# Kernel optimization log

Measured on AMD Instinct MI355X. Metric: run time of the kernel, lower is better.

The kernel has to match this reference:

```python
import jax, jax.numpy as jnp
import numpy as np

B, T, E, NH = 2, 1024, 512, 8


def setup_inputs() -> dict:
    key = jax.random.key(0)
    ks = jax.random.split(key, 7)
    s = 0.02
    return {
        "x": jax.random.normal(ks[0], (B, T, E), dtype=jnp.float32),
        "W_qkv": jax.random.normal(ks[1], (E, 3 * E), dtype=jnp.float32) * s,
        "b_qkv": jax.random.normal(ks[2], (3 * E,), dtype=jnp.float32) * s,
        "W_od": jax.random.normal(ks[3], (E, 2 * NH), dtype=jnp.float32) * s,
        "b_od": jax.random.normal(ks[4], (2 * NH,), dtype=jnp.float32) * s,
        "W_out": jax.random.normal(ks[5], (E, E), dtype=jnp.float32) * s,
        "b_out": jax.random.normal(ks[6], (E,), dtype=jnp.float32) * s,
        "length": T,
    }


def reference(x, W_qkv, b_qkv, W_od, b_od, W_out, b_out, length):
    b, t, e = x.shape
    nh = W_od.shape[1] // 2
    hd = e // nh
    scaling = float(hd) ** (-0.5)

    qkv = x @ W_qkv + b_qkv
    Q, K, V = jnp.split(qkv, 3, axis=-1)  # each (b, t, e)

    od = Q @ W_od + b_od  # (b, t, 2*nh)
    offset, duration = jnp.split(od, 2, axis=-1)
    offset = jnp.tanh(offset) * length
    duration = jax.nn.sigmoid(duration) * length

    qidx = jnp.arange(length, dtype=x.dtype)[None, :, None]  # (1, t, 1)
    anchor = qidx + offset  # (b, t, nh)

    # 'b t nh -> (b nh) t'
    anchor = anchor.transpose(0, 2, 1).reshape(b * nh, t)
    duration = duration.transpose(0, 2, 1).reshape(b * nh, t)

    start = anchor - duration
    end = anchor + duration
    bl = jnp.floor(start)          # left bound index
    br = jnp.ceil(end)             # right bound index
    al = jnp.floor(anchor)         # anchor left index
    ar = al + 1                    # anchor right index
    dist_al = anchor - al          # anchor_dist_l

    r = jnp.arange(length, dtype=x.dtype)[None, None, :]  # (1, 1, t)

    def pmask(idx):  # point mask (bnh, t, t), float
        return (r == idx[:, :, None]).astype(x.dtype)

    point_weight = (1.0
                    + (bl - start)[:, :, None] * pmask(bl)
                    + (end - br)[:, :, None] * pmask(br)
                    + dist_al[:, :, None] * pmask(ar)
                    + (1.0 - dist_al)[:, :, None] * pmask(al))

    attn_mask = (r < bl[:, :, None]) | (r > br[:, :, None])  # (bnh, t, t) bool

    def heads(z):  # 'b t (nh hd) -> (b nh) t hd'
        return z.reshape(b, t, nh, hd).transpose(0, 2, 1, 3).reshape(b * nh, t, hd)

    Qh, Kh, Vh = heads(Q), heads(K), heads(V)

    scores = jnp.einsum('bic,brc->bir', Qh, Kh) * scaling
    scores = scores * point_weight
    scores = jnp.where(attn_mask, jnp.asarray(-1e8, x.dtype), scores)
    attn = jax.nn.softmax(scores, axis=-1)

    out = jnp.einsum('bir,brc->bic', attn, Vh)  # (bnh, t, hd)
    out = out.reshape(b, nh, t, hd).transpose(0, 2, 1, 3).reshape(b, t, e)
    return out @ W_out + b_out
```

## Files before the change

### kernel.cpp

```cpp
#include <hip/hip_runtime.h>

typedef unsigned short ushort_t;
typedef short s16x8 __attribute__((ext_vector_type(8)));
typedef float f32x4 __attribute__((ext_vector_type(4)));

#define DEVINL __device__ __forceinline__

DEVINL ushort_t f2b(float f) {
  union { float f; unsigned int u; } v; v.f = f;
  unsigned int r = (v.u + 0x7fffu + ((v.u >> 16) & 1u)) >> 16;
  return (ushort_t)r;
}

DEVINL ushort_t f2b_hw(float f) {
  union { __bf16 h; ushort_t u; } cv;
  cv.h = (__bf16)f;
  return cv.u;
}

__global__ __launch_bounds__(256) void prep_kernel(
    const float* __restrict__ Wqkv, const float* __restrict__ bq,
    const float* __restrict__ Wod, const float* __restrict__ bod,
    const float* __restrict__ Wout,
    ushort_t* __restrict__ WqkvT, ushort_t* __restrict__ WoT,
    float* __restrict__ Wcomb, float* __restrict__ bcomb)
{
  __shared__ ushort_t tile[64 * 72];
  const int b = blockIdx.x;
  const int tid = threadIdx.x;

  if (b < 256) {
    const float* in;
    ushort_t* out;
    int N, bx, by;
    if (b < 192) { in = Wqkv; out = WqkvT; N = 1536; bx = b % 24; by = b / 24; }
    else         { in = Wout; out = WoT;   N = 512;  bx = (b - 192) % 8; by = (b - 192) / 8; }
    const int K = 512;
    const int n0 = bx * 64, k0 = by * 64;
    const int cr = tid >> 4;
    const int cc = (tid & 15) * 4;
#pragma unroll
    for (int p = 0; p < 4; p++) {
      int k = k0 + p * 16 + cr;
      float4 v = *(const float4*)(in + k * N + n0 + cc);
      ushort4 o; o.x = f2b(v.x); o.y = f2b(v.y); o.z = f2b(v.z); o.w = f2b(v.w);
      *(ushort4*)(tile + (p * 16 + cr) * 72 + cc) = o;
    }
    __syncthreads();
#pragma unroll
    for (int p = 0; p < 4; p++) {
      int n = n0 + p * 16 + cr;
      ushort4 v;
      v.x = tile[(cc + 0) * 72 + p * 16 + cr];
      v.y = tile[(cc + 1) * 72 + p * 16 + cr];
      v.z = tile[(cc + 2) * 72 + p * 16 + cr];
      v.w = tile[(cc + 3) * 72 + p * 16 + cr];
      *(ushort4*)(out + n * K + k0 + cc) = v;
    }
    return;
  }

  const int w = tid >> 6, lane = tid & 63;
  const int c = (b - 256) * 4 + w;
  if (c > 512) return;
  float a[8];
  const float* src = (c < 512) ? (Wqkv + c * 1536 + lane * 8) : (bq + lane * 8);
  float4 a0 = *(const float4*)(src);
  float4 a1 = *(const float4*)(src + 4);
  a[0]=a0.x; a[1]=a0.y; a[2]=a0.z; a[3]=a0.w;
  a[4]=a1.x; a[5]=a1.y; a[6]=a1.z; a[7]=a1.w;

  float s[16];
#pragma unroll
  for (int j = 0; j < 16; j++) s[j] = 0.f;
#pragma unroll
  for (int i = 0; i < 8; i++) {
    const float* wp = Wod + (lane * 8 + i) * 16;
#pragma unroll
    for (int j = 0; j < 16; j++) s[j] += a[i] * wp[j];
  }
#pragma unroll
  for (int mask = 1; mask < 64; mask <<= 1)
#pragma unroll
    for (int j = 0; j < 16; j++) s[j] += __shfl_xor(s[j], mask);

  if (lane < 16) {
    if (c < 512) Wcomb[c * 16 + lane] = s[lane];
    else         bcomb[lane] = s[lane] + bod[lane];
  }
}

__global__ __launch_bounds__(256) void od_kernel(
    const float* __restrict__ x, const float* __restrict__ Wcomb,
    const float* __restrict__ bcomb, const int* __restrict__ lenp,
    float* __restrict__ params, ushort_t* __restrict__ xb)
{
  const int w = threadIdx.x >> 6, lane = threadIdx.x & 63;
  const int m = blockIdx.x * 4 + w;
  int li = lenp[0];
  float len = (li > 0 && li < 1048576) ? (float)li : 1024.0f;

  const float* qp = x + m * 512 + lane * 8;
  float q[8];
  float4 qa = *(const float4*)(qp);
  float4 qb = *(const float4*)(qp + 4);
  q[0]=qa.x; q[1]=qa.y; q[2]=qa.z; q[3]=qa.w;
  q[4]=qb.x; q[5]=qb.y; q[6]=qb.z; q[7]=qb.w;

  s16x8 ov;
#pragma unroll
  for (int i = 0; i < 8; i++) ov[i] = (short)f2b(q[i]);
  *(s16x8*)(xb + m * 512 + lane * 8) = ov;

  float s[16];
#pragma unroll
  for (int j = 0; j < 16; j++) s[j] = 0.f;
#pragma unroll
  for (int i = 0; i < 8; i++) {
    const float* wp = Wcomb + (lane * 8 + i) * 16;
#pragma unroll
    for (int j = 0; j < 16; j++) s[j] += q[i] * wp[j];
  }
#pragma unroll
  for (int mask = 1; mask < 64; mask <<= 1)
#pragma unroll
    for (int j = 0; j < 16; j++) s[j] += __shfl_xor(s[j], mask);

  if (lane < 8) {
    int h = lane;
    int bb = m >> 10, t = m & 1023;
    float odo = s[h] + bcomb[h];
    float odd = s[8 + h] + bcomb[8 + h];
    float offset = tanhf(odo) * len;
    float dur = len / (1.f + expf(-odd));
    float anchor = (float)t + offset;
    float start = anchor - dur, end = anchor + dur;
    float bl = floorf(start), br = ceilf(end);
    float al = floorf(anchor);
    float da = anchor - al;
    float* pp = params + ((bb * 8 + h) * 1024 + t) * 6;
    pp[0] = bl; pp[1] = br; pp[2] = al;
    pp[3] = bl - start; pp[4] = end - br; pp[5] = da;
  }
}

__global__ __launch_bounds__(256) void qkv_gemm_kernel(
    const ushort_t* __restrict__ xb, const ushort_t* __restrict__ WT,
    const float* __restrict__ bqkv,
    ushort_t* __restrict__ Qh, ushort_t* __restrict__ Kh, ushort_t* __restrict__ VT)
{
  __shared__ ushort_t As[64 * 32];
  __shared__ ushort_t Bs[128 * 32];
  const int tid = threadIdx.x;
  const int lane = tid & 63, w = tid >> 6;
  const int wr = w >> 1, wc = w & 1;
  const int quad = lane >> 4, l16 = lane & 15;
  const int m0 = blockIdx.y * 64, n0 = blockIdx.x * 128;

  f32x4 acc[2][4];
#pragma unroll
  for (int i = 0; i < 2; i++)
#pragma unroll
    for (int j = 0; j < 4; j++) acc[i][j] = f32x4{0.f, 0.f, 0.f, 0.f};

  const int idx = tid * 8;
  const int ra = idx >> 5, ca = idx & 31;
  const int rb1 = (idx + 2048) >> 5, cb1 = (idx + 2048) & 31;

  for (int k0 = 0; k0 < 512; k0 += 32) {
    s16x8 va  = *(const s16x8*)(xb + (m0 + ra) * 512 + k0 + ca);
    s16x8 vb0 = *(const s16x8*)(WT + (n0 + ra) * 512 + k0 + ca);
    s16x8 vb1 = *(const s16x8*)(WT + (n0 + rb1) * 512 + k0 + cb1);
    __syncthreads();
    *(s16x8*)(As + idx) = va;
    *(s16x8*)(Bs + idx) = vb0;
    *(s16x8*)(Bs + idx + 2048) = vb1;
    __syncthreads();

    s16x8 af[2], bfr[4];
#pragma unroll
    for (int mt = 0; mt < 2; mt++)
      af[mt] = *(const s16x8*)(As + (wr * 32 + mt * 16 + l16) * 32 + quad * 8);
#pragma unroll
    for (int nt = 0; nt < 4; nt++)
      bfr[nt] = *(const s16x8*)(Bs + (wc * 64 + nt * 16 + l16) * 32 + quad * 8);
#pragma unroll
    for (int mt = 0; mt < 2; mt++)
#pragma unroll
      for (int nt = 0; nt < 4; nt++)
        acc[mt][nt] = __builtin_amdgcn_mfma_f32_16x16x32_bf16(af[mt], bfr[nt], acc[mt][nt], 0, 0, 0);
  }

#pragma unroll
  for (int nt = 0; nt < 4; nt++) {
    int c = n0 + wc * 64 + nt * 16 + l16;
    float bias = bqkv[c];
    int which = c >> 9;
    int e = c & 511;
    int h = e >> 6, d = e & 63;
#pragma unroll
    for (int mt = 0; mt < 2; mt++) {
      int mbase = m0 + wr * 32 + mt * 16 + quad * 4;
      int bb = mbase >> 10, t = mbase & 1023;
      int bh = bb * 8 + h;
      if (which == 2) {
        ushort4 pk;
        pk.x = f2b(acc[mt][nt][0] + bias);
        pk.y = f2b(acc[mt][nt][1] + bias);
        pk.z = f2b(acc[mt][nt][2] + bias);
        pk.w = f2b(acc[mt][nt][3] + bias);
        *(ushort4*)(VT + (bh * 64 + d) * 1024 + t) = pk;
      } else {
        ushort_t* dst = (which == 0) ? Qh : Kh;
        float sc = (which == 0) ? 0.125f : 1.0f;
#pragma unroll
        for (int rr = 0; rr < 4; rr++)
          dst[(bh * 1024 + t + rr) * 64 + d] = f2b((acc[mt][nt][rr] + bias) * sc);
      }
    }
  }
}

__global__ __launch_bounds__(256, 3) void attn_kernel(
    const ushort_t* __restrict__ Qh, const ushort_t* __restrict__ Kh,
    const ushort_t* __restrict__ VT, const float* __restrict__ params,
    ushort_t* __restrict__ Oh)
{
  __shared__ ushort_t Kt[64 * 72 + 32];
  __shared__ ushort_t Vt[64 * 72 + 96];
  __shared__ ushort_t Ps[4][16 * 40];
  __shared__ float Om[4][16][65];
  __shared__ float lwS[4][16];

  const int tid = threadIdx.x;
  const int lane = tid & 63, w = tid >> 6;
  const int quad = lane >> 4, l16 = lane & 15;
  const int bh = blockIdx.x;
  const int mrow = blockIdx.y * 16;
  ushort_t* Pw = Ps[w];

#pragma unroll
  for (int rr = 0; rr < 4; rr++)
    Pw[(quad * 4 + rr) * 40 + 16 + l16] = 0;

  s16x8 aq0 = *(const s16x8*)(Qh + (bh * 1024 + mrow + l16) * 64 + quad * 8);
  s16x8 aq1 = *(const s16x8*)(Qh + (bh * 1024 + mrow + l16) * 64 + 32 + quad * 8);

  float bl[4], br[4], al[4], wl[4], wr2[4], da[4];
  float lo = 1.0e9f, hi = -1.0e9f;
#pragma unroll
  for (int rr = 0; rr < 4; rr++) {
    int row = mrow + quad * 4 + rr;
    const float* pp = params + (bh * 1024 + row) * 6;
    bl[rr] = pp[0]; br[rr] = pp[1]; al[rr] = pp[2];
    wl[rr] = pp[3]; wr2[rr] = pp[4]; da[rr] = pp[5];
    bool empty = (br[rr] < 0.f) || (bl[rr] > 1023.f);
    float lo_r = empty ? 0.f    : fmaxf(bl[rr], 0.f);
    float hi_r = empty ? 1023.f : fminf(br[rr], 1023.f);
    lo = fminf(lo, lo_r); hi = fmaxf(hi, hi_r);
  }
  lo = fminf(lo, __shfl_xor(lo, 16));
  lo = fminf(lo, __shfl_xor(lo, 32));
  hi = fmaxf(hi, __shfl_xor(hi, 16));
  hi = fmaxf(hi, __shfl_xor(hi, 32));
  const int tlo = ((int)lo) >> 6, thi = ((int)hi) >> 6;

  float lr[4] = {0.f, 0.f, 0.f, 0.f};
  f32x4 Oacc[4];
#pragma unroll
  for (int nt = 0; nt < 4; nt++) Oacc[nt] = f32x4{0.f, 0.f, 0.f, 0.f};

  const int srow = tid >> 2, sseg = (tid & 3) * 16;
  const ushort_t* kgb = Kh + (bh * 1024 + srow) * 64 + sseg;
  const ushort_t* vgb = VT + (bh * 64 + srow) * 1024 + sseg;

  s16x8 kr0, kr1, vr0, vr1;
  {
    const int r0 = tlo * 64;
    kr0 = *(const s16x8*)(kgb + r0 * 64);
    kr1 = *(const s16x8*)(kgb + r0 * 64 + 8);
    vr0 = *(const s16x8*)(vgb + r0);
    vr1 = *(const s16x8*)(vgb + r0 + 8);
  }

  for (int tt = tlo; tt <= thi; tt++) {
    const int r0 = tt * 64;
    __syncthreads();
    *(s16x8*)(Kt + srow * 72 + sseg)     = kr0;
    *(s16x8*)(Kt + srow * 72 + sseg + 8) = kr1;
    *(s16x8*)(Vt + srow * 72 + sseg)     = vr0;
    *(s16x8*)(Vt + srow * 72 + sseg + 8) = vr1;
    __syncthreads();

    if (tt + 1 <= thi) {
      const int r1 = (tt + 1) * 64;
      kr0 = *(const s16x8*)(kgb + r1 * 64);
      kr1 = *(const s16x8*)(kgb + r1 * 64 + 8);
      vr0 = *(const s16x8*)(vgb + r1);
      vr1 = *(const s16x8*)(vgb + r1 + 8);
    }

    s16x8 bk0 = *(const s16x8*)(Kt + (w * 16 + l16) * 72 + quad * 8);
    s16x8 bk1 = *(const s16x8*)(Kt + (w * 16 + l16) * 72 + 32 + quad * 8);
    f32x4 S = {0.f, 0.f, 0.f, 0.f};
    S = __builtin_amdgcn_mfma_f32_16x16x32_bf16(aq0, bk0, S, 0, 0, 0);
    S = __builtin_amdgcn_mfma_f32_16x16x32_bf16(aq1, bk1, S, 0, 0, 0);

    const float cf = (float)(r0 + w * 16 + l16);
    const float c0f = (float)(r0 + w * 16), c1f = c0f + 15.f;
    bool fastb = true;
#pragma unroll
    for (int rr = 0; rr < 4; rr++) {
      bool f = (bl[rr] < c0f) && (br[rr] > c1f) &&
               ((al[rr] + 1.f < c0f) || (al[rr] > c1f));
      fastb = fastb && f;
    }
    float p4[4];
    if (__all((int)fastb)) {
#pragma unroll
      for (int rr = 0; rr < 4; rr++) {
        float p = __expf(S[rr]);
        lr[rr] += p;
        p4[rr] = p;
      }
    } else {
#pragma unroll
      for (int rr = 0; rr < 4; rr++) {
        float s = S[rr];
        float wgt = 1.f;
        wgt += (cf == bl[rr]) ? wl[rr] : 0.f;
        wgt += (cf == br[rr]) ? wr2[rr] : 0.f;
        wgt += (cf == al[rr] + 1.f) ? da[rr] : 0.f;
        wgt += (cf == al[rr]) ? (1.f - da[rr]) : 0.f;
        s *= wgt;
        s = (cf < bl[rr] || cf > br[rr]) ? -30.f : s;
        float p = __expf(s);
        lr[rr] += p;
        p4[rr] = p;
      }
    }

#pragma unroll
    for (int rr = 0; rr < 4; rr++)
      Pw[(quad * 4 + rr) * 40 + l16] = f2b_hw(p4[rr]);

    s16x8 pa = *(const s16x8*)(Pw + l16 * 40 + quad * 8);
#pragma unroll
    for (int nt = 0; nt < 4; nt++) {
      s16x8 bv = *(const s16x8*)(Vt + (nt * 16 + l16) * 72 + w * 16 + quad * 8);
      Oacc[nt] = __builtin_amdgcn_mfma_f32_16x16x32_bf16(pa, bv, Oacc[nt], 0, 0, 0);
    }
  }

#pragma unroll
  for (int mask = 1; mask < 16; mask <<= 1)
#pragma unroll
    for (int rr = 0; rr < 4; rr++) lr[rr] += __shfl_xor(lr[rr], mask);

#pragma unroll
  for (int nt = 0; nt < 4; nt++)
#pragma unroll
    for (int rr = 0; rr < 4; rr++)
      Om[w][quad * 4 + rr][nt * 16 + l16] = Oacc[nt][rr];
  if (l16 == 0) {
#pragma unroll
    for (int rr = 0; rr < 4; rr++) lwS[w][quad * 4 + rr] = lr[rr];
  }
  __syncthreads();

  {
    const int col = tid & 63;
    const int rbase = (tid >> 6) * 4;
    const int bb = bh >> 3, h = bh & 7;
#pragma unroll
    for (int k = 0; k < 4; k++) {
      int r = rbase + k;
      float lg = lwS[0][r] + lwS[1][r] + lwS[2][r] + lwS[3][r];
      float o  = Om[0][r][col] + Om[1][r][col] + Om[2][r][col] + Om[3][r][col];
      int t = mrow + r;
      Oh[((bb << 10) + t) * 512 + h * 64 + col] = f2b_hw(o / lg);
    }
  }
}

__global__ __launch_bounds__(256) void out_gemm_kernel(
    const ushort_t* __restrict__ Oh, const ushort_t* __restrict__ WT,
    const float* __restrict__ bout, float* __restrict__ outp)
{
  __shared__ ushort_t As[64 * 32];
  __shared__ ushort_t Bs[64 * 32];
  const int tid = threadIdx.x;
  const int lane = tid & 63, w = tid >> 6;
  const int wr = w >> 1, wc = w & 1;
  const int quad = lane >> 4, l16 = lane & 15;
  const int m0 = blockIdx.y * 64, n0 = blockIdx.x * 64;

  f32x4 acc[2][2];
#pragma unroll
  for (int i = 0; i < 2; i++)
#pragma unroll
    for (int j = 0; j < 2; j++) acc[i][j] = f32x4{0.f, 0.f, 0.f, 0.f};

  const int idx = tid * 8;
  const int ra = idx >> 5, ca = idx & 31;

  for (int k0 = 0; k0 < 512; k0 += 32) {
    s16x8 va = *(const s16x8*)(Oh + (m0 + ra) * 512 + k0 + ca);
    s16x8 vb = *(const s16x8*)(WT + (n0 + ra) * 512 + k0 + ca);
    __syncthreads();
    *(s16x8*)(As + idx) = va;
    *(s16x8*)(Bs + idx) = vb;
    __syncthreads();

    s16x8 af[2], bfr[2];
#pragma unroll
    for (int mt = 0; mt < 2; mt++)
      af[mt] = *(const s16x8*)(As + (wr * 32 + mt * 16 + l16) * 32 + quad * 8);
#pragma unroll
    for (int nt = 0; nt < 2; nt++)
      bfr[nt] = *(const s16x8*)(Bs + (wc * 32 + nt * 16 + l16) * 32 + quad * 8);
#pragma unroll
    for (int mt = 0; mt < 2; mt++)
#pragma unroll
      for (int nt = 0; nt < 2; nt++)
        acc[mt][nt] = __builtin_amdgcn_mfma_f32_16x16x32_bf16(af[mt], bfr[nt], acc[mt][nt], 0, 0, 0);
  }

#pragma unroll
  for (int nt = 0; nt < 2; nt++) {
    int c = n0 + wc * 32 + nt * 16 + l16;
    float bias = bout[c];
#pragma unroll
    for (int mt = 0; mt < 2; mt++) {
#pragma unroll
      for (int rr = 0; rr < 4; rr++) {
        int m = m0 + wr * 32 + mt * 16 + quad * 4 + rr;
        outp[m * 512 + c] = acc[mt][nt][rr] + bias;
      }
    }
  }
}

extern "C" void kernel_launch(void* const* d_in, const int* in_sizes, int n_in,
                              void* d_out, int out_size, void* d_ws, size_t ws_size,
                              hipStream_t stream)
{
  const float* x    = (const float*)d_in[0];
  const float* Wqkv = (const float*)d_in[1];
  const float* bqkv = (const float*)d_in[2];
  const float* Wod  = (const float*)d_in[3];
  const float* bod  = (const float*)d_in[4];
  const float* Wout = (const float*)d_in[5];
  const float* bout = (const float*)d_in[6];
  const int* lenp   = (const int*)d_in[7];

  char* ws = (char*)d_ws;
  ushort_t* WqkvT  = (ushort_t*)(ws);
  ushort_t* WoT    = (ushort_t*)(ws + 1572864);
  ushort_t* xb     = (ushort_t*)(ws + 2097152);
  ushort_t* Qh     = (ushort_t*)(ws + 4194304);
  ushort_t* Kh     = (ushort_t*)(ws + 6291456);
  ushort_t* VT     = (ushort_t*)(ws + 8388608);
  ushort_t* Oh     = (ushort_t*)(ws + 10485760);
  float*    Wcomb  = (float*)(ws + 12582912);
  float*    bcomb  = (float*)(ws + 12615680);
  float*    params = (float*)(ws + 12615744);

  prep_kernel<<<385, 256, 0, stream>>>(Wqkv, bqkv, Wod, bod, Wout, WqkvT, WoT, Wcomb, bcomb);
  od_kernel<<<512, 256, 0, stream>>>(x, Wcomb, bcomb, lenp, params, xb);
  qkv_gemm_kernel<<<dim3(12, 32), 256, 0, stream>>>(xb, WqkvT, bqkv, Qh, Kh, VT);
  attn_kernel<<<dim3(16, 64), 256, 0, stream>>>(Qh, Kh, VT, params, Oh);
  out_gemm_kernel<<<dim3(8, 32), 256, 0, stream>>>(Oh, WoT, bout, (float*)d_out);
}
```

Before: 129.9 us.

## Double-buffer K/V tiles and process 32 query rows per attention block

```diff
diff --git a/kernel.cpp b/kernel.cpp
--- a/kernel.cpp
+++ b/kernel.cpp
@@ -226,31 +226,27 @@
     const ushort_t* __restrict__ VT, const float* __restrict__ params,
     ushort_t* __restrict__ Oh)
 {
-  __shared__ ushort_t Kt[64 * 72 + 32];
-  __shared__ ushort_t Vt[64 * 72 + 96];
+  constexpr int TS = 64 * 72;
+  __shared__ __align__(16) ushort_t KV[4 * TS];
   __shared__ ushort_t Ps[4][16 * 40];
-  __shared__ float Om[4][16][65];
-  __shared__ float lwS[4][16];
+  __shared__ float loS[4], hiS[4];
 
   const int tid = threadIdx.x;
   const int lane = tid & 63, w = tid >> 6;
+  const int wr = w >> 1, wc = w & 1;
   const int quad = lane >> 4, l16 = lane & 15;
   const int bh = blockIdx.x;
-  const int mrow = blockIdx.y * 16;
+  const int mrow = blockIdx.y * 32;
   ushort_t* Pw = Ps[w];
 
-#pragma unroll
-  for (int rr = 0; rr < 4; rr++)
-    Pw[(quad * 4 + rr) * 40 + 16 + l16] = 0;
-
-  s16x8 aq0 = *(const s16x8*)(Qh + (bh * 1024 + mrow + l16) * 64 + quad * 8);
-  s16x8 aq1 = *(const s16x8*)(Qh + (bh * 1024 + mrow + l16) * 64 + 32 + quad * 8);
+  s16x8 aq0 = *(const s16x8*)(Qh + (bh * 1024 + mrow + wr * 16 + l16) * 64 + quad * 8);
+  s16x8 aq1 = *(const s16x8*)(Qh + (bh * 1024 + mrow + wr * 16 + l16) * 64 + 32 + quad * 8);
 
   float bl[4], br[4], al[4], wl[4], wr2[4], da[4];
   float lo = 1.0e9f, hi = -1.0e9f;
 #pragma unroll
   for (int rr = 0; rr < 4; rr++) {
-    int row = mrow + quad * 4 + rr;
+    int row = mrow + wr * 16 + quad * 4 + rr;
     const float* pp = params + (bh * 1024 + row) * 6;
     bl[rr] = pp[0]; br[rr] = pp[1]; al[rr] = pp[2];
     wl[rr] = pp[3]; wr2[rr] = pp[4]; da[rr] = pp[5];
@@ -263,6 +259,10 @@
   lo = fminf(lo, __shfl_xor(lo, 32));
   hi = fmaxf(hi, __shfl_xor(hi, 16));
   hi = fmaxf(hi, __shfl_xor(hi, 32));
+  if (lane == 0) { loS[w] = lo; hiS[w] = hi; }
+  __syncthreads();
+  lo = fminf(fminf(loS[0], loS[1]), fminf(loS[2], loS[3]));
+  hi = fmaxf(fmaxf(hiS[0], hiS[1]), fmaxf(hiS[2], hiS[3]));
   const int tlo = ((int)lo) >> 6, thi = ((int)hi) >> 6;
 
   float lr[4] = {0.f, 0.f, 0.f, 0.f};
@@ -282,17 +282,24 @@
     vr0 = *(const s16x8*)(vgb + r0);
     vr1 = *(const s16x8*)(vgb + r0 + 8);
   }
-
-  for (int tt = tlo; tt <= thi; tt++) {
-    const int r0 = tt * 64;
-    __syncthreads();
+  {
+    ushort_t* Kt = KV;
+    ushort_t* Vt = KV + TS;
     *(s16x8*)(Kt + srow * 72 + sseg)     = kr0;
     *(s16x8*)(Kt + srow * 72 + sseg + 8) = kr1;
     *(s16x8*)(Vt + srow * 72 + sseg)     = vr0;
     *(s16x8*)(Vt + srow * 72 + sseg + 8) = vr1;
-    __syncthreads();
-
-    if (tt + 1 <= thi) {
+  }
+  __syncthreads();
+
+  for (int tt = tlo; tt <= thi; tt++) {
+    const int p = (tt - tlo) & 1;
+    ushort_t* Ktp = KV + p * 2 * TS;
+    ushort_t* Vtp = KV + p * 2 * TS + TS;
+    const int r0 = tt * 64;
+    const bool more = (tt + 1 <= thi);
+
+    if (more) {
       const int r1 = (tt + 1) * 64;
       kr0 = *(const s16x8*)(kgb + r1 * 64);
       kr1 = *(const s16x8*)(kgb + r1 * 64 + 8);
@@ -300,14 +307,20 @@
       vr1 = *(const s16x8*)(vgb + r1 + 8);
     }
 
-    s16x8 bk0 = *(const s16x8*)(Kt + (w * 16 + l16) * 72 + quad * 8);
-    s16x8 bk1 = *(const s16x8*)(Kt + (w * 16 + l16) * 72 + 32 + quad * 8);
-    f32x4 S = {0.f, 0.f, 0.f, 0.f};
-    S = __builtin_amdgcn_mfma_f32_16x16x32_bf16(aq0, bk0, S, 0, 0, 0);
-    S = __builtin_amdgcn_mfma_f32_16x16x32_bf16(aq1, bk1, S, 0, 0, 0);
-
-    const float cf = (float)(r0 + w * 16 + l16);
-    const float c0f = (float)(r0 + w * 16), c1f = c0f + 15.f;
+    f32x4 S[2];
+#pragma unroll
+    for (int ng = 0; ng < 2; ng++) {
+      const ushort_t* kp = Ktp + (wc * 32 + ng * 16 + l16) * 72 + quad * 8;
+      s16x8 bk0 = *(const s16x8*)(kp);
+      s16x8 bk1 = *(const s16x8*)(kp + 32);
+      f32x4 z = {0.f, 0.f, 0.f, 0.f};
+      z = __builtin_amdgcn_mfma_f32_16x16x32_bf16(aq0, bk0, z, 0, 0, 0);
+      z = __builtin_amdgcn_mfma_f32_16x16x32_bf16(aq1, bk1, z, 0, 0, 0);
+      S[ng] = z;
+    }
+
+    const int cbase = r0 + wc * 32;
+    const float c0f = (float)cbase, c1f = c0f + 31.f;
     bool fastb = true;
 #pragma unroll
     for (int rr = 0; rr < 4; rr++) {
@@ -315,71 +328,89 @@
                ((al[rr] + 1.f < c0f) || (al[rr] > c1f));
       fastb = fastb && f;
     }
-    float p4[4];
+    float p8[2][4];
     if (__all((int)fastb)) {
 #pragma unroll
-      for (int rr = 0; rr < 4; rr++) {
-        float p = __expf(S[rr]);
-        lr[rr] += p;
-        p4[rr] = p;
+      for (int ng = 0; ng < 2; ng++)
+#pragma unroll
+        for (int rr = 0; rr < 4; rr++) {
+          float pv = __expf(S[ng][rr]);
+          lr[rr] += pv;
+          p8[ng][rr] = pv;
+        }
+    } else {
+#pragma unroll
+      for (int ng = 0; ng < 2; ng++) {
+        const float cf = (float)(cbase + ng * 16 + l16);
+#pragma unroll
+        for (int rr = 0; rr < 4; rr++) {
+          float s = S[ng][rr];
+          float wgt = 1.f;
+          wgt += (cf == bl[rr]) ? wl[rr] : 0.f;
+          wgt += (cf == br[rr]) ? wr2[rr] : 0.f;
+          wgt += (cf == al[rr] + 1.f) ? da[rr] : 0.f;
+          wgt += (cf == al[rr]) ? (1.f - da[rr]) : 0.f;
+          s *= wgt;
+          s = (cf < bl[rr] || cf > br[rr]) ? -30.f : s;
+          float pv = __expf(s);
+          lr[rr] += pv;
+          p8[ng][rr] = pv;
+        }
       }
-    } else {
-#pragma unroll
-      for (int rr = 0; rr < 4; rr++) {
-        float s = S[rr];
-        float wgt = 1.f;
-        wgt += (cf == bl[rr]) ? wl[rr] : 0.f;
-        wgt += (cf == br[rr]) ? wr2[rr] : 0.f;
-        wgt += (cf == al[rr] + 1.f) ? da[rr] : 0.f;
-        wgt += (cf == al[rr]) ? (1.f - da[rr]) : 0.f;
-        s *= wgt;
-        s = (cf < bl[rr] || cf > br[rr]) ? -30.f : s;
-        float p = __expf(s);
-        lr[rr] += p;
-        p4[rr] = p;
-      }
-    }
-
+    }
+
+#pragma unroll
+    for (int ng = 0; ng < 2; ng++)
+#pragma unroll
+      for (int rr = 0; rr < 4; rr++)
+        Pw[(quad * 4 + rr) * 40 + ng * 16 + l16] = f2b_hw(p8[ng][rr]);
+
+    s16x8 pa = *(const s16x8*)(Pw + l16 * 40 + quad * 8);
+
+#pragma unroll
+    for (int nt = 0; nt < 4; nt++) {
+      s16x8 bv = *(const s16x8*)(Vtp + (nt * 16 + l16) * 72 + wc * 32 + quad * 8);
+      Oacc[nt] = __builtin_amdgcn_mfma_f32_16x16x32_bf16(pa, bv, Oacc[nt], 0, 0, 0);
+    }
+
+    if (more) {
+      ushort_t* Ktn = KV + (p ^ 1) * 2 * TS;
+      ushort_t* Vtn = KV + (p ^ 1) * 2 * TS + TS;
+      *(s16x8*)(Ktn + srow * 72 + sseg)     = kr0;
+      *(s16x8*)(Ktn + srow * 72 + sseg + 8) = kr1;
+      *(s16x8*)(Vtn + srow * 72 + sseg)     = vr0;
+      *(s16x8*)(Vtn + srow * 72 + sseg + 8) = vr1;
+      __syncthreads();
+    }
+  }
+
+#pragma unroll
+  for (int mask = 1; mask < 16; mask <<= 1)
+#pragma unroll
+    for (int rr = 0; rr < 4; rr++) lr[rr] += __shfl_xor(lr[rr], mask);
+
+  __syncthreads();
+  float* Om  = (float*)KV;
+  float* lwf = Om + 2 * 32 * 65;
+  const int rloc = wr * 16 + quad * 4;
+#pragma unroll
+  for (int nt = 0; nt < 4; nt++)
 #pragma unroll
     for (int rr = 0; rr < 4; rr++)
-      Pw[(quad * 4 + rr) * 40 + l16] = f2b_hw(p4[rr]);
-
-    s16x8 pa = *(const s16x8*)(Pw + l16 * 40 + quad * 8);
-#pragma unroll
-    for (int nt = 0; nt < 4; nt++) {
-      s16x8 bv = *(const s16x8*)(Vt + (nt * 16 + l16) * 72 + w * 16 + quad * 8);
-      Oacc[nt] = __builtin_amdgcn_mfma_f32_16x16x32_bf16(pa, bv, Oacc[nt], 0, 0, 0);
-    }
-  }
-
-#pragma unroll
-  for (int mask = 1; mask < 16; mask <<= 1)
-#pragma unroll
-    for (int rr = 0; rr < 4; rr++) lr[rr] += __shfl_xor(lr[rr], mask);
-
-#pragma unroll
-  for (int nt = 0; nt < 4; nt++)
-#pragma unroll
-    for (int rr = 0; rr < 4; rr++)
-      Om[w][quad * 4 + rr][nt * 16 + l16] = Oacc[nt][rr];
+      Om[(wc * 32 + rloc + rr) * 65 + nt * 16 + l16] = Oacc[nt][rr];
   if (l16 == 0) {
 #pragma unroll
-    for (int rr = 0; rr < 4; rr++) lwS[w][quad * 4 + rr] = lr[rr];
+    for (int rr = 0; rr < 4; rr++) lwf[wc * 32 + rloc + rr] = lr[rr];
   }
   __syncthreads();
 
-  {
-    const int col = tid & 63;
-    const int rbase = (tid >> 6) * 4;
-    const int bb = bh >> 3, h = bh & 7;
-#pragma unroll
-    for (int k = 0; k < 4; k++) {
-      int r = rbase + k;
-      float lg = lwS[0][r] + lwS[1][r] + lwS[2][r] + lwS[3][r];
-      float o  = Om[0][r][col] + Om[1][r][col] + Om[2][r][col] + Om[3][r][col];
-      int t = mrow + r;
-      Oh[((bb << 10) + t) * 512 + h * 64 + col] = f2b_hw(o / lg);
-    }
+  const int bb = bh >> 3, h = bh & 7;
+  for (int e = tid; e < 2048; e += 256) {
+    int r = e >> 6, col = e & 63;
+    float lg = lwf[r] + lwf[32 + r];
+    float o  = Om[r * 65 + col] + Om[(32 + r) * 65 + col];
+    int t = mrow + r;
+    Oh[((bb << 10) + t) * 512 + h * 64 + col] = f2b_hw(o / lg);
   }
 }
 
@@ -469,6 +500,6 @@
   prep_kernel<<<385, 256, 0, stream>>>(Wqkv, bqkv, Wod, bod, Wout, WqkvT, WoT, Wcomb, bcomb);
   od_kernel<<<512, 256, 0, stream>>>(x, Wcomb, bcomb, lenp, params, xb);
   qkv_gemm_kernel<<<dim3(12, 32), 256, 0, stream>>>(xb, WqkvT, bqkv, Qh, Kh, VT);
-  attn_kernel<<<dim3(16, 64), 256, 0, stream>>>(Qh, Kh, VT, params, Oh);
+  attn_kernel<<<dim3(16, 32), 256, 0, stream>>>(Qh, Kh, VT, params, Oh);
   out_gemm_kernel<<<dim3(8, 32), 256, 0, stream>>>(Oh, WoT, bout, (float*)d_out);
 }
```

New measurement: 129.3 us. No clear change (-0.4%).
